# Performance work log

Measured on AMD Instinct MI355X. Metric: run time of the kernel, lower is better.

The kernel has to match this reference:

```python
import jax, jax.numpy as jnp
import numpy as np

B, N = 4, 20                        # batch, qubits
L = int(np.ceil(np.log2(N)))        # 5 layers, one 4x4 generator each


def setup_inputs():
    key = jax.random.key(0)
    k1, k2, k3, k4 = jax.random.split(key, 4)
    psi_re = jax.random.normal(k1, (B, 2 ** N), dtype=jnp.float32)
    psi_im = jax.random.normal(k2, (B, 2 ** N), dtype=jnp.float32)
    nrm = jnp.sqrt(jnp.sum(psi_re ** 2 + psi_im ** 2, axis=1, keepdims=True))
    psi_re, psi_im = psi_re / nrm, psi_im / nrm   # normalized quantum state
    H_re = jax.random.normal(k3, (L, 4, 4), dtype=jnp.float32)
    H_im = jax.random.normal(k4, (L, 4, 4), dtype=jnp.float32)
    return {"psi_re": psi_re, "psi_im": psi_im, "H_re": H_re, "H_im": H_im}


def _make_unitary(A):
    # torch.matrix_exp(A - A^H): expm of an anti-Hermitian generator via eigh
    G = A - A.conj().T
    w, V = jnp.linalg.eigh(-1j * G)            # G = i * Hermitian
    return (V * jnp.exp(1j * w)) @ V.conj().T  # expm(G), unitary


def _apply_gate(T, U4, axes):
    # contract 4x4 gate (reshaped [2,2,2,2]) onto two qubit axes of tensor T
    T = jnp.tensordot(U4, T, axes=((2, 3), axes))
    return jnp.moveaxis(T, (0, 1), axes)


def _gate_pairs(nq):
    pairs = [(2 * i, 2 * i + 1) for i in range(nq // 2)]
    if nq > 2:
        pairs += [(2 * i + 1, (2 * i + 2) % nq) for i in range(nq // 2)]
    return pairs


def _forward(psi_re, psi_im, H_re, H_im):
    psi = (psi_re + 1j * psi_im).astype(jnp.complex64).reshape((B,) + (2,) * N)
    H = (H_re + 1j * H_im).astype(jnp.complex64)
    state, is_dm, nq = psi, False, N
    for layer in range(L):
        U = _make_unitary(H[layer]).reshape(2, 2, 2, 2)
        Uc = U.conj()
        # _2local_conv: brick pattern of the same 2-qubit gate
        for (a, b) in _gate_pairs(nq):
            state = _apply_gate(state, U, (1 + a, 1 + b))
            if is_dm:  # density matrix: also apply U* on bra axes
                state = _apply_gate(state, Uc, (1 + nq + a, 1 + nq + b))
        # _2local_pool: measuring qubits 0..nq//2-1 with index shifting removes
        # the even-indexed qubits -> partial trace over them
        if nq >= 2:
            traced = [2 * i for i in range(nq // 2)]
            kept = [q for q in range(nq) if q not in traced]
            t, k = len(traced), len(kept)
            if is_dm:
                perm = (0,) + tuple(1 + q for q in kept) + tuple(1 + q for q in traced) \
                     + tuple(1 + nq + q for q in kept) + tuple(1 + nq + q for q in traced)
                r = jnp.transpose(state, perm).reshape(B, 2 ** k, 2 ** t, 2 ** k, 2 ** t)
                state = jnp.einsum('bitjt->bij', r).reshape((B,) + (2,) * k + (2,) * k)
            else:
                perm = (0,) + tuple(1 + q for q in traced) + tuple(1 + q for q in kept)
                p = jnp.transpose(state, perm).reshape(B, 2 ** t, 2 ** k)
                state = jnp.einsum('bti,btj->bij', p, p.conj()).reshape((B,) + (2,) * k + (2,) * k)
                is_dm = True
            nq = k
    # final state.measure(0): reduced 1-qubit density matrix, take P(outcome 0)
    r = state.reshape(B, 2, 2 ** (nq - 1), 2, 2 ** (nq - 1))
    rho0 = jnp.einsum('birjr->bij', r)
    return rho0[:, 0, 0].real


def reference(psi_re, psi_im, H_re, H_im):
    return _forward(psi_re, psi_im, H_re, H_im)
```

## Files before the change

kernel.cpp:

```cpp
#include <hip/hip_runtime.h>
#include <math.h>


typedef float cpx __attribute__((ext_vector_type(2)));

__device__ __forceinline__ cpx mkc(float x, float y) { cpx r; r.x = x; r.y = y; return r; }

__device__ __forceinline__ cpx cmul(cpx a, cpx b) {
  cpx r = a.xx * b;
  return __builtin_elementwise_fma(mkc(-a.y, a.y), b.yx, r);
}
__device__ __forceinline__ cpx cmadd(cpx acc, cpx a, cpx b) {
  acc = __builtin_elementwise_fma(a.xx, b, acc);
  return __builtin_elementwise_fma(mkc(-a.y, a.y), b.yx, acc);
}
__device__ __forceinline__ cpx cmaddc(cpx acc, cpx a, cpx b) {
  acc = __builtin_elementwise_fma(a.xx, mkc(b.x, -b.y), acc);
  return __builtin_elementwise_fma(a.yy, b.yx, acc);
}

__device__ __forceinline__ int pad(int e) { return e + (e >> 4); }
__device__ __forceinline__ int ins(int x, int p) {
  return ((x >> p) << (p + 1)) | (x & ((1 << p) - 1));
}

#define S_STR 36
#define T_STR 1153

__device__ __forceinline__ void gate4(cpx& v0, cpx& v1, cpx& v2, cpx& v3,
                                      const cpx (&U)[16]) {
  cpx n0 = cmul(U[0], v0);  n0 = cmadd(n0, U[1], v1);  n0 = cmadd(n0, U[2], v2);  n0 = cmadd(n0, U[3], v3);
  cpx n1 = cmul(U[4], v0);  n1 = cmadd(n1, U[5], v1);  n1 = cmadd(n1, U[6], v2);  n1 = cmadd(n1, U[7], v3);
  cpx n2 = cmul(U[8], v0);  n2 = cmadd(n2, U[9], v1);  n2 = cmadd(n2, U[10], v2); n2 = cmadd(n2, U[11], v3);
  cpx n3 = cmul(U[12], v0); n3 = cmadd(n3, U[13], v1); n3 = cmadd(n3, U[14], v2); n3 = cmadd(n3, U[15], v3);
  v0 = n0; v1 = n1; v2 = n2; v3 = n3;
}

template <int NG>
__device__ __forceinline__ void gate16n(cpx (&v)[16], const cpx (&U)[16]) {
#pragma unroll
  for (int g = 0; g < 4; g++)
    gate4(v[g * 4 + 0], v[g * 4 + 1], v[g * 4 + 2], v[g * 4 + 3], U);
#pragma unroll
  for (int lo = 0; lo < 4; lo++)
    gate4(v[lo], v[lo + 4], v[lo + 8], v[lo + 12], U);
  if (NG == 3) {
#pragma unroll
    for (int b3 = 0; b3 < 2; b3++)
#pragma unroll
      for (int b0 = 0; b0 < 2; b0++) {
        int j = b3 * 8 + b0;
        gate4(v[j], v[j + 2], v[j + 4], v[j + 6], U);
      }
  }
}

__device__ __forceinline__ void apply_gate_tile13(cpx* t, const cpx (&U)[16],
                                                  int pa, int pb, int tid) {
  int p0 = pa < pb ? pa : pb;
  int p1 = pa < pb ? pb : pa;
  int m0 = (1 << p0) - 1, m1 = (1 << p1) - 1;
  int ia = 1 << pa, ib = 1 << pb;
#pragma unroll
  for (int g = tid; g < 2048; g += 512) {
    int idx = ((g & ~m0) << 1) | (g & m0);
    idx = ((idx & ~m1) << 1) | (idx & m1);
    int e0 = pad(idx), e1 = pad(idx | ib), e2 = pad(idx | ia), e3 = pad(idx | ia | ib);
    cpx v0 = t[e0], v1 = t[e1], v2 = t[e2], v3 = t[e3];
    gate4(v0, v1, v2, v3, U);
    t[e0] = v0; t[e1] = v1; t[e2] = v2; t[e3] = v3;
  }
}

template <int NG>
__device__ __forceinline__ void phase4_f(cpx* t, const cpx (&U)[16],
                                         int q0, int q1, int q2, int q3,
                                         int o0, int o1, int o2, int o3, int tid) {
  int idx = ins(ins(ins(ins(tid, q0), q1), q2), q3);
  cpx v[16];
#pragma unroll
  for (int j = 0; j < 16; j++) {
    int off = ((j & 1) ? o0 : 0) + ((j & 2) ? o1 : 0) + ((j & 4) ? o2 : 0) + ((j & 8) ? o3 : 0);
    v[j] = t[pad(idx + off)];
  }
  gate16n<NG>(v, U);
#pragma unroll
  for (int j = 0; j < 16; j++) {
    int off = ((j & 1) ? o0 : 0) + ((j & 2) ? o1 : 0) + ((j & 4) ? o2 : 0) + ((j & 8) ? o3 : 0);
    t[pad(idx + off)] = v[j];
  }
}

template <int NG>
__device__ __forceinline__ void phase4_pool(cpx* w, const cpx (&U)[16],
                                            int a_lo, int a_hi, int c_lo, int c_hi,
                                            int o0, int o1, int o2, int o3, int tid) {
  int uu = tid & 7, ss = (tid >> 3) & 7, t_lo = tid >> 6;
  int u = ins(ins(uu, a_lo), a_hi);
  int s = ins(ins(ss, c_lo), c_hi);
  int base = t_lo * T_STR + s * S_STR + u;
  cpx v[16];
#pragma unroll
  for (int j = 0; j < 16; j++) {
    int off = ((j & 1) ? o0 : 0) + ((j & 2) ? o1 : 0) + ((j & 4) ? o2 : 0) + ((j & 8) ? o3 : 0);
    v[j] = w[base + off];
  }
  gate16n<NG>(v, U);
#pragma unroll
  for (int j = 0; j < 16; j++) {
    int off = ((j & 1) ? o0 : 0) + ((j & 2) ? o1 : 0) + ((j & 4) ? o2 : 0) + ((j & 8) ? o3 : 0);
    w[base + off] = v[j];
  }
}

__device__ __forceinline__ void pool_p3(cpx* w, const cpx (&U)[16], int tid) {
#pragma unroll
  for (int it = 0; it < 2; it++) {
    int h = tid + it * 512;
    int t_lo = h & 7, ss = (h >> 3) & 15, uu = (h >> 7) & 7;
    int base = t_lo * T_STR + (ss << 1) * S_STR + (uu << 2);
    cpx v[8];
    v[0] = w[base];          v[1] = w[base + 1];
    v[4] = w[base + 2];      v[5] = w[base + 3];
    v[2] = w[base + S_STR];      v[3] = w[base + S_STR + 1];
    v[6] = w[base + S_STR + 2];  v[7] = w[base + S_STR + 3];
    gate4(v[0], v[1], v[2], v[3], U);
    gate4(v[4], v[5], v[6], v[7], U);
    gate4(v[0], v[2], v[4], v[6], U);
    gate4(v[1], v[3], v[5], v[7], U);
    w[base] = v[0];          w[base + 1] = v[1];
    w[base + 2] = v[4];      w[base + 3] = v[5];
    w[base + S_STR] = v[2];      w[base + S_STR + 1] = v[3];
    w[base + S_STR + 2] = v[6];  w[base + S_STR + 3] = v[7];
  }
}

__device__ __forceinline__ cpx expm16(const float* __restrict__ Hre,
                                      const float* __restrict__ Him,
                                      int l, int l16) {
  int r = l16 >> 2, c = l16 & 3;
  double tr = (double)Hre[l * 16 + r * 4 + c] - (double)Hre[l * 16 + c * 4 + r];
  double ti = (double)Him[l * 16 + r * 4 + c] + (double)Him[l * 16 + c * 4 + r];
  double a = sqrt(tr * tr + ti * ti);
  a += __shfl_xor(a, 1, 16);
  a += __shfl_xor(a, 2, 16);
  double nrm = fmax(a, __shfl_xor(a, 4, 16));
  nrm = fmax(nrm, __shfl_xor(nrm, 8, 16));
  int s = 0;
  while (nrm > 0.25 && s < 60) { nrm *= 0.5; s++; }
  double sc = ldexp(1.0, -s);
  tr *= sc; ti *= sc;
  double id = (r == c) ? 1.0 : 0.0;
  double er = id, ei = 0.0, pr = id, pi = 0.0;
  for (int k = 1; k <= 16; k++) {
    double qr = 0.0, qi = 0.0;
#pragma unroll
    for (int m = 0; m < 4; m++) {
      double pmr = __shfl(pr, r * 4 + m, 16);
      double pmi = __shfl(pi, r * 4 + m, 16);
      double tmr = __shfl(tr, m * 4 + c, 16);
      double tmi = __shfl(ti, m * 4 + c, 16);
      qr = fma(pmr, tmr, fma(-pmi, tmi, qr));
      qi = fma(pmr, tmi, fma(pmi, tmr, qi));
    }
    double inv = 1.0 / (double)k;
    pr = qr * inv; pi = qi * inv;
    er += pr; ei += pi;
  }
  for (int it = 0; it < s; it++) {
    double qr = 0.0, qi = 0.0;
#pragma unroll
    for (int m = 0; m < 4; m++) {
      double amr = __shfl(er, r * 4 + m, 16);
      double ami = __shfl(ei, r * 4 + m, 16);
      double bmr = __shfl(er, m * 4 + c, 16);
      double bmi = __shfl(ei, m * 4 + c, 16);
      qr = fma(amr, bmr, fma(-ami, bmi, qr));
      qi = fma(amr, bmi, fma(ami, bmr, qi));
    }
    er = qr; ei = qi;
  }
  return mkc((float)er, (float)ei);
}

__global__ __launch_bounds__(256, 4) void l0_pass1(const float* __restrict__ pre,
                                                   const float* __restrict__ pim,
                                                   const float* __restrict__ Hre,
                                                   const float* __restrict__ Him,
                                                   cpx* __restrict__ Umat,
                                                   cpx* __restrict__ state) {
  extern __shared__ cpx tile[];
  __shared__ cpx Ush[16];
  int tid = threadIdx.x;
  int bid = blockIdx.x;
  int b = bid >> 8, hi = bid & 255;
  size_t base = ((size_t)b << 20) | ((size_t)hi << 12);
  for (int e4 = tid; e4 < 1024; e4 += 256) {
    int e = e4 << 2;
    float4 re = *(const float4*)&pre[base + e];
    float4 im = *(const float4*)&pim[base + e];
    int d = pad(e);
    tile[d] = mkc(re.x, im.x);
    tile[d + 1] = mkc(re.y, im.y);
    tile[d + 2] = mkc(re.z, im.z);
    tile[d + 3] = mkc(re.w, im.w);
  }
  {
    int wv = tid >> 6, g16 = (tid & 63) >> 4, l16 = tid & 15;
    int layer = (wv == 0) ? g16 : ((wv == 1 && g16 == 0) ? 4 : -1);
    if (layer == 0 || (bid == 0 && layer > 0)) {
      cpx ue = expm16(Hre, Him, layer, l16);
      if (layer == 0) Ush[l16] = ue;
      if (bid == 0) Umat[layer * 16 + l16] = ue;
    }
  }
  __syncthreads();
  cpx U[16];
#pragma unroll
  for (int k = 0; k < 16; k++) U[k] = Ush[k];
  phase4_f<3>(tile, U, 0, 1, 2, 3, 1, 2, 4, 8, tid);            __syncthreads();
  phase4_f<3>(tile, U, 4, 5, 6, 7, 16, 32, 64, 128, tid);       __syncthreads();
  phase4_f<3>(tile, U, 8, 9, 10, 11, 256, 512, 1024, 2048, tid);__syncthreads();
  phase4_f<2>(tile, U, 3, 4, 7, 8, 8, 16, 128, 256, tid);       __syncthreads();
  int hifix = ((hi & 1) << 4) | (((hi >> 1) & 1) << 16) | (((hi >> 2) & 1) << 6)
            | (((hi >> 3) & 1) << 17) | (((hi >> 4) & 1) << 5) | (((hi >> 5) & 1) << 18)
            | (((hi >> 6) & 1) << 7) | (((hi >> 7) & 1) << 19);
  size_t dbase = ((size_t)b << 20) | (unsigned)hifix;
  for (int e4 = tid; e4 < 1024; e4 += 256) {
    int le = e4;
    int d = ((le & 1) << 2) | (((le >> 1) & 1) << 3) | (((le >> 2) & 1) << 8)
          | (((le >> 3) & 1) << 12) | (((le >> 4) & 1) << 10) | (((le >> 5) & 1) << 13)
          | (((le >> 6) & 1) << 9) | (((le >> 7) & 1) << 14) | (((le >> 8) & 1) << 11)
          | (((le >> 9) & 1) << 15);
    int src = pad(e4 << 2);
    cpx x0 = tile[src], x1 = tile[src + 1], x2 = tile[src + 2], x3 = tile[src + 3];
    float4* dst = (float4*)&state[dbase + d];
    dst[0] = make_float4(x0.x, x0.y, x1.x, x1.y);
    dst[1] = make_float4(x2.x, x2.y, x3.x, x3.y);
  }
}

__global__ __launch_bounds__(512, 4) void l0_pass2(const cpx* __restrict__ Umat,
                                                   cpx* __restrict__ state) {
  extern __shared__ cpx tile[];
  int tid = threadIdx.x;
  int bid = blockIdx.x;
  int b = bid >> 7, mid = bid & 127;
  size_t base = ((size_t)b << 20) | ((size_t)mid << 8);
  cpx U[16];
#pragma unroll
  for (int k = 0; k < 16; k++) U[k] = Umat[k];
  for (int f = tid; f < 4096; f += 512) {
    int run = f >> 7, idx = f & 127;
    size_t a = base + ((size_t)run << 15) + ((size_t)idx << 1);
    float4 v = *(const float4*)&state[a];
    int d = pad(run * 256 + idx * 2);
    tile[d] = mkc(v.x, v.y);
    tile[d + 1] = mkc(v.z, v.w);
  }
  __syncthreads();
  phase4_f<3>(tile, U, 4, 6, 9, 10, 16, 512, 64, 1024, tid);    __syncthreads();
  phase4_f<3>(tile, U, 5, 7, 11, 12, 32, 2048, 128, 4096, tid); __syncthreads();
  phase4_f<2>(tile, U, 4, 5, 8, 10, 256, 16, 1024, 32, tid);    __syncthreads();
  apply_gate_tile13(tile, U, 0, 12, tid);                       __syncthreads();
  for (int f = tid; f < 4096; f += 512) {
    int run = f >> 7, idx = f & 127;
    size_t a = base + ((size_t)run << 15) + ((size_t)idx << 1);
    int d = pad(run * 256 + idx * 2);
    cpx x0 = tile[d], x1 = tile[d + 1];
    *(float4*)&state[a] = make_float4(x0.x, x0.y, x1.x, x1.y);
  }
}

__global__ __launch_bounds__(512, 4) void pool_l1(const cpx* __restrict__ Umat,
                                                  const cpx* __restrict__ state,
                                                  float4* __restrict__ partial) {
  extern __shared__ cpx w[];
  int tid = threadIdx.x;
  int bid = blockIdx.x;
  int b = bid >> 7, thi = bid & 127;
  size_t base = ((size_t)b << 20) | ((size_t)thi << 13);
  cpx U[16];
#pragma unroll
  for (int k = 0; k < 16; k++) U[k] = Umat[16 + k];
  for (int f = tid; f < 4096; f += 512) {
    int e = f << 1;
    float4 v = *(const float4*)&state[base + e];
    int u = (((e >> 8) & 1) << 1) | (((e >> 9) & 1) << 2) | (((e >> 4) & 1) << 3) | (((e >> 5) & 1) << 4);
    int s = ((e >> 2) & 1) | (((e >> 10) & 1) << 1) | (((e >> 11) & 1) << 2)
          | (((e >> 6) & 1) << 3) | (((e >> 7) & 1) << 4);
    int t = ((e >> 1) & 1) | (((e >> 3) & 1) << 1) | (((e >> 12) & 1) << 2);
    int c = t * T_STR + s * S_STR + u;
    w[c] = mkc(v.x, v.y);
    w[c + 1] = mkc(v.z, v.w);
  }
  __syncthreads();
  phase4_pool<3>(w, U, 3, 4, 3, 4, 8, 8 * S_STR, 16, 16 * S_STR, tid); __syncthreads();
  phase4_pool<3>(w, U, 1, 2, 1, 2, 2, 2 * S_STR, 4, 4 * S_STR, tid);   __syncthreads();
  pool_p3(w, U, tid);                                                  __syncthreads();
  phase4_pool<2>(w, U, 0, 3, 2, 4, 4 * S_STR, 8, 16 * S_STR, 1, tid);  __syncthreads();
  int wv = tid >> 6, lane = tid & 63;
  int u0 = (lane >> 3) << 2, v0 = (lane & 7) << 2;
  cpx acc[4][4];
#pragma unroll
  for (int i = 0; i < 4; i++)
#pragma unroll
    for (int j = 0; j < 4; j++) acc[i][j] = mkc(0.f, 0.f);
  {
    int tb = wv * T_STR;
#pragma unroll 4
    for (int s = 0; s < 32; s++) {
      int row = tb + s * S_STR;
      cpx x[4], y[4];
#pragma unroll
      for (int i = 0; i < 4; i++) { x[i] = w[row + u0 + i]; y[i] = w[row + v0 + i]; }
#pragma unroll
      for (int i = 0; i < 4; i++)
#pragma unroll
        for (int j = 0; j < 4; j++) acc[i][j] = cmaddc(acc[i][j], x[i], y[j]);
    }
  }
  __syncthreads();
#pragma unroll
  for (int i = 0; i < 4; i++)
#pragma unroll
    for (int j = 0; j < 4; j++)
      w[wv * 1024 + (u0 + i) * 32 + (v0 + j)] = acc[i][j];
  __syncthreads();
  {
    cpx s0 = mkc(0.f, 0.f), s1 = mkc(0.f, 0.f);
#pragma unroll
    for (int k = 0; k < 8; k++) {
      s0 += w[k * 1024 + 2 * tid];
      s1 += w[k * 1024 + 2 * tid + 1];
    }
    partial[((size_t)bid << 9) | tid] = make_float4(s0.x, s0.y, s1.x, s1.y);
  }
}

__global__ __launch_bounds__(256) void finish(const cpx* __restrict__ Umat,
                                              const float4* __restrict__ accv,
                                              float* __restrict__ out) {
  __shared__ cpx rho[1024];
  __shared__ cpx r3s[64];
  __shared__ cpx r4s[16];
  int tid = threadIdx.x;
  int b = blockIdx.x;
  float4* rf = (float4*)rho;
  for (int f = tid; f < 512; f += 256) {
    float4 acc = make_float4(0.f, 0.f, 0.f, 0.f);
#pragma unroll 8
    for (int h = 0; h < 128; h++) {
      float4 v = accv[(size_t)(b * 128 + h) * 512 + f];
      acc.x += v.x; acc.y += v.y; acc.z += v.z; acc.w += v.w;
    }
    rf[f] = acc;
  }
  __syncthreads();

  cpx U[16], Uc[16];
#pragma unroll
  for (int k = 0; k < 16; k++) { U[k] = Umat[32 + k]; Uc[k] = mkc(U[k].x, -U[k].y); }
  const int gl2[4][2] = {{4,3},{2,1},{3,2},{1,0}};
#pragma unroll
  for (int gi = 0; gi < 4; gi++) {
    int pa = gl2[gi][0], pb = gl2[gi][1];
    int p0 = pa < pb ? pa : pb, p1 = pa < pb ? pb : pa;
    int m0 = (1 << p0) - 1, m1 = (1 << p1) - 1;
    int ia = 1 << pa, ib = 1 << pb;
    {
      int j = tid >> 3, g = tid & 7;
      int idx = ((g & ~m0) << 1) | (g & m0);
      idx = ((idx & ~m1) << 1) | (idx & m1);
      cpx v0 = rho[idx * 32 + j], v1 = rho[(idx | ib) * 32 + j];
      cpx v2 = rho[(idx | ia) * 32 + j], v3 = rho[(idx | ia | ib) * 32 + j];
      gate4(v0, v1, v2, v3, U);
      rho[idx * 32 + j] = v0; rho[(idx | ib) * 32 + j] = v1;
      rho[(idx | ia) * 32 + j] = v2; rho[(idx | ia | ib) * 32 + j] = v3;
    }
    __syncthreads();
    {
      int i = tid >> 3, g = tid & 7;
      int idx = ((g & ~m0) << 1) | (g & m0);
      idx = ((idx & ~m1) << 1) | (idx & m1);
      cpx v0 = rho[i * 32 + idx], v1 = rho[i * 32 + (idx | ib)];
      cpx v2 = rho[i * 32 + (idx | ia)], v3 = rho[i * 32 + (idx | ia | ib)];
      gate4(v0, v1, v2, v3, Uc);
      rho[i * 32 + idx] = v0; rho[i * 32 + (idx | ib)] = v1;
      rho[i * 32 + (idx | ia)] = v2; rho[i * 32 + (idx | ia | ib)] = v3;
    }
    __syncthreads();
  }
  if (tid < 64) {
    int u = tid >> 3, v = tid & 7;
    cpx acc = mkc(0.f, 0.f);
#pragma unroll
    for (int s = 0; s < 4; s++) {
      int iu = ((s >> 1) << 4) | ((u >> 2) << 3) | ((s & 1) << 2) | (((u >> 1) & 1) << 1) | (u & 1);
      int iv = ((s >> 1) << 4) | ((v >> 2) << 3) | ((s & 1) << 2) | (((v >> 1) & 1) << 1) | (v & 1);
      cpx x = rho[iu * 32 + iv];
      acc.x += x.x; acc.y += x.y;
    }
    r3s[u * 8 + v] = acc;
  }
  __syncthreads();

#pragma unroll
  for (int k = 0; k < 16; k++) { U[k] = Umat[48 + k]; Uc[k] = mkc(U[k].x, -U[k].y); }
  const int gl3[2][2] = {{2,1},{1,0}};
#pragma unroll
  for (int gi = 0; gi < 2; gi++) {
    int pa = gl3[gi][0], pb = gl3[gi][1];
    int p0 = pa < pb ? pa : pb, p1 = pa < pb ? pb : pa;
    int m0 = (1 << p0) - 1, m1 = (1 << p1) - 1;
    int ia = 1 << pa, ib = 1 << pb;
    if (tid < 16) {
      int j = tid >> 1, g = tid & 1;
      int idx = ((g & ~m0) << 1) | (g & m0);
      idx = ((idx & ~m1) << 1) | (idx & m1);
      cpx v0 = r3s[idx * 8 + j], v1 = r3s[(idx | ib) * 8 + j];
      cpx v2 = r3s[(idx | ia) * 8 + j], v3 = r3s[(idx | ia | ib) * 8 + j];
      gate4(v0, v1, v2, v3, U);
      r3s[idx * 8 + j] = v0; r3s[(idx | ib) * 8 + j] = v1;
      r3s[(idx | ia) * 8 + j] = v2; r3s[(idx | ia | ib) * 8 + j] = v3;
    }
    __syncthreads();
    if (tid < 16) {
      int i = tid >> 1, g = tid & 1;
      int idx = ((g & ~m0) << 1) | (g & m0);
      idx = ((idx & ~m1) << 1) | (idx & m1);
      cpx v0 = r3s[i * 8 + idx], v1 = r3s[i * 8 + (idx | ib)];
      cpx v2 = r3s[i * 8 + (idx | ia)], v3 = r3s[i * 8 + (idx | ia | ib)];
      gate4(v0, v1, v2, v3, Uc);
      r3s[i * 8 + idx] = v0; r3s[i * 8 + (idx | ib)] = v1;
      r3s[i * 8 + (idx | ia)] = v2; r3s[i * 8 + (idx | ia | ib)] = v3;
    }
    __syncthreads();
  }
  if (tid < 16) {
    int u = tid >> 2, v = tid & 3;
    cpx acc = mkc(0.f, 0.f);
#pragma unroll
    for (int s = 0; s < 2; s++) {
      cpx x = r3s[((s << 2) | u) * 8 + ((s << 2) | v)];
      acc.x += x.x; acc.y += x.y;
    }
    r4s[u * 4 + v] = acc;
  }
  __syncthreads();

#pragma unroll
  for (int k = 0; k < 16; k++) { U[k] = Umat[64 + k]; Uc[k] = mkc(U[k].x, -U[k].y); }
  if (tid < 4) {
    int j = tid;
    cpx v0 = r4s[0 * 4 + j], v1 = r4s[1 * 4 + j], v2 = r4s[2 * 4 + j], v3 = r4s[3 * 4 + j];
    gate4(v0, v1, v2, v3, U);
    r4s[0 * 4 + j] = v0; r4s[1 * 4 + j] = v1; r4s[2 * 4 + j] = v2; r4s[3 * 4 + j] = v3;
  }
  __syncthreads();
  if (tid < 4) {
    int i = tid;
    cpx v0 = r4s[i * 4 + 0], v1 = r4s[i * 4 + 1], v2 = r4s[i * 4 + 2], v3 = r4s[i * 4 + 3];
    gate4(v0, v1, v2, v3, Uc);
    r4s[i * 4 + 0] = v0; r4s[i * 4 + 1] = v1; r4s[i * 4 + 2] = v2; r4s[i * 4 + 3] = v3;
  }
  __syncthreads();
  if (tid == 0) out[b] = r4s[0].x + r4s[10].x;
}

extern "C" void kernel_launch(void* const* d_in, const int* in_sizes, int n_in,
                              void* d_out, int out_size, void* d_ws, size_t ws_size,
                              hipStream_t stream) {
  const float* psi_re = (const float*)d_in[0];
  const float* psi_im = (const float*)d_in[1];
  const float* H_re = (const float*)d_in[2];
  const float* H_im = (const float*)d_in[3];
  float* out = (float*)d_out;

  char* ws = (char*)d_ws;
  cpx* Umat = (cpx*)ws;
  cpx* state = (cpx*)(ws + 4096);
  float4* partial = (float4*)(ws + 4096 + ((size_t)1 << 25));

  const size_t LDS_P1 = 4352 * sizeof(cpx);
  const size_t LDS_L0 = 8704 * sizeof(cpx);
  const size_t LDS_POOL = 8 * T_STR * sizeof(cpx);

  hipLaunchKernelGGL(l0_pass1, dim3(1024), dim3(256), LDS_P1, stream,
                     psi_re, psi_im, H_re, H_im, Umat, state);
  hipLaunchKernelGGL(l0_pass2, dim3(512), dim3(512), LDS_L0, stream,
                     (const cpx*)Umat, state);
  hipLaunchKernelGGL(pool_l1, dim3(512), dim3(512), LDS_POOL, stream,
                     (const cpx*)Umat, (const cpx*)state, partial);
  hipLaunchKernelGGL(finish, dim3(4), dim3(256), 0, stream,
                     (const cpx*)Umat, (const float4*)partial, out);
}
```

Before: 175.5 us.

## Enlarge pass1 tiles to 8K elements and batch global loads before LDS stores

l0_pass1 now handles 8192-element tiles with 512 threads instead of 4096 with 256, so the grid halves and the output bit permutation gains one more tile-local bit. Across all three big kernels, the global loads are first gathered into register arrays and then written to LDS (likewise on the stores), which raises memory-level parallelism per thread. The cost is higher register pressure and, in pass1, a doubled LDS footprint that may cut occupancy.

Result: slower. 183.0 us (+4.3%).

```diff
diff --git a/kernel.cpp b/kernel.cpp
--- a/kernel.cpp
+++ b/kernel.cpp
@@ -183,7 +183,7 @@
   return mkc((float)er, (float)ei);
 }
 
-__global__ __launch_bounds__(256, 4) void l0_pass1(const float* __restrict__ pre,
+__global__ __launch_bounds__(512, 4) void l0_pass1(const float* __restrict__ pre,
                                                    const float* __restrict__ pim,
                                                    const float* __restrict__ Hre,
                                                    const float* __restrict__ Him,
@@ -193,17 +193,23 @@
   __shared__ cpx Ush[16];
   int tid = threadIdx.x;
   int bid = blockIdx.x;
-  int b = bid >> 8, hi = bid & 255;
-  size_t base = ((size_t)b << 20) | ((size_t)hi << 12);
-  for (int e4 = tid; e4 < 1024; e4 += 256) {
-    int e = e4 << 2;
-    float4 re = *(const float4*)&pre[base + e];
-    float4 im = *(const float4*)&pim[base + e];
+  int b = bid >> 7, hi = bid & 127;
+  size_t base = ((size_t)b << 20) | ((size_t)hi << 13);
+  float4 re[4], im[4];
+#pragma unroll
+  for (int k = 0; k < 4; k++) {
+    int e = (tid + (k << 9)) << 2;
+    re[k] = *(const float4*)&pre[base + e];
+    im[k] = *(const float4*)&pim[base + e];
+  }
+#pragma unroll
+  for (int k = 0; k < 4; k++) {
+    int e = (tid + (k << 9)) << 2;
     int d = pad(e);
-    tile[d] = mkc(re.x, im.x);
-    tile[d + 1] = mkc(re.y, im.y);
-    tile[d + 2] = mkc(re.z, im.z);
-    tile[d + 3] = mkc(re.w, im.w);
+    tile[d]     = mkc(re[k].x, im[k].x);
+    tile[d + 1] = mkc(re[k].y, im[k].y);
+    tile[d + 2] = mkc(re[k].z, im[k].z);
+    tile[d + 3] = mkc(re[k].w, im[k].w);
   }
   {
     int wv = tid >> 6, g16 = (tid & 63) >> 4, l16 = tid & 15;
@@ -222,21 +228,27 @@
   phase4_f<3>(tile, U, 4, 5, 6, 7, 16, 32, 64, 128, tid);       __syncthreads();
   phase4_f<3>(tile, U, 8, 9, 10, 11, 256, 512, 1024, 2048, tid);__syncthreads();
   phase4_f<2>(tile, U, 3, 4, 7, 8, 8, 16, 128, 256, tid);       __syncthreads();
-  int hifix = ((hi & 1) << 4) | (((hi >> 1) & 1) << 16) | (((hi >> 2) & 1) << 6)
-            | (((hi >> 3) & 1) << 17) | (((hi >> 4) & 1) << 5) | (((hi >> 5) & 1) << 18)
-            | (((hi >> 6) & 1) << 7) | (((hi >> 7) & 1) << 19);
+  int hifix = ((hi & 1) << 16) | (((hi >> 1) & 1) << 6) | (((hi >> 2) & 1) << 17)
+            | (((hi >> 3) & 1) << 5) | (((hi >> 4) & 1) << 18) | (((hi >> 5) & 1) << 7)
+            | (((hi >> 6) & 1) << 19);
   size_t dbase = ((size_t)b << 20) | (unsigned)hifix;
-  for (int e4 = tid; e4 < 1024; e4 += 256) {
-    int le = e4;
+  cpx x[16];
+#pragma unroll
+  for (int k = 0; k < 4; k++) {
+    int src = pad((tid + (k << 9)) << 2);
+    x[4 * k + 0] = tile[src];     x[4 * k + 1] = tile[src + 1];
+    x[4 * k + 2] = tile[src + 2]; x[4 * k + 3] = tile[src + 3];
+  }
+#pragma unroll
+  for (int k = 0; k < 4; k++) {
+    int le = tid + (k << 9);
     int d = ((le & 1) << 2) | (((le >> 1) & 1) << 3) | (((le >> 2) & 1) << 8)
           | (((le >> 3) & 1) << 12) | (((le >> 4) & 1) << 10) | (((le >> 5) & 1) << 13)
           | (((le >> 6) & 1) << 9) | (((le >> 7) & 1) << 14) | (((le >> 8) & 1) << 11)
-          | (((le >> 9) & 1) << 15);
-    int src = pad(e4 << 2);
-    cpx x0 = tile[src], x1 = tile[src + 1], x2 = tile[src + 2], x3 = tile[src + 3];
+          | (((le >> 9) & 1) << 15) | (((le >> 10) & 1) << 4);
     float4* dst = (float4*)&state[dbase + d];
-    dst[0] = make_float4(x0.x, x0.y, x1.x, x1.y);
-    dst[1] = make_float4(x2.x, x2.y, x3.x, x3.y);
+    dst[0] = make_float4(x[4 * k].x, x[4 * k].y, x[4 * k + 1].x, x[4 * k + 1].y);
+    dst[1] = make_float4(x[4 * k + 2].x, x[4 * k + 2].y, x[4 * k + 3].x, x[4 * k + 3].y);
   }
 }
 
@@ -250,25 +262,43 @@
   cpx U[16];
 #pragma unroll
   for (int k = 0; k < 16; k++) U[k] = Umat[k];
-  for (int f = tid; f < 4096; f += 512) {
-    int run = f >> 7, idx = f & 127;
-    size_t a = base + ((size_t)run << 15) + ((size_t)idx << 1);
-    float4 v = *(const float4*)&state[a];
-    int d = pad(run * 256 + idx * 2);
-    tile[d] = mkc(v.x, v.y);
-    tile[d + 1] = mkc(v.z, v.w);
+  {
+    float4 v[8];
+#pragma unroll
+    for (int k = 0; k < 8; k++) {
+      int f = tid + (k << 9);
+      int run = f >> 7, idx = f & 127;
+      v[k] = *(const float4*)&state[base + ((size_t)run << 15) + ((size_t)idx << 1)];
+    }
+#pragma unroll
+    for (int k = 0; k < 8; k++) {
+      int f = tid + (k << 9);
+      int d = pad((f >> 7) * 256 + (f & 127) * 2);
+      tile[d] = mkc(v[k].x, v[k].y);
+      tile[d + 1] = mkc(v[k].z, v[k].w);
+    }
   }
   __syncthreads();
   phase4_f<3>(tile, U, 4, 6, 9, 10, 16, 512, 64, 1024, tid);    __syncthreads();
   phase4_f<3>(tile, U, 5, 7, 11, 12, 32, 2048, 128, 4096, tid); __syncthreads();
   phase4_f<2>(tile, U, 4, 5, 8, 10, 256, 16, 1024, 32, tid);    __syncthreads();
   apply_gate_tile13(tile, U, 0, 12, tid);                       __syncthreads();
-  for (int f = tid; f < 4096; f += 512) {
-    int run = f >> 7, idx = f & 127;
-    size_t a = base + ((size_t)run << 15) + ((size_t)idx << 1);
-    int d = pad(run * 256 + idx * 2);
-    cpx x0 = tile[d], x1 = tile[d + 1];
-    *(float4*)&state[a] = make_float4(x0.x, x0.y, x1.x, x1.y);
+  {
+    cpx y[16];
+#pragma unroll
+    for (int k = 0; k < 8; k++) {
+      int f = tid + (k << 9);
+      int d = pad((f >> 7) * 256 + (f & 127) * 2);
+      y[2 * k] = tile[d];
+      y[2 * k + 1] = tile[d + 1];
+    }
+#pragma unroll
+    for (int k = 0; k < 8; k++) {
+      int f = tid + (k << 9);
+      int run = f >> 7, idx = f & 127;
+      size_t a = base + ((size_t)run << 15) + ((size_t)idx << 1);
+      *(float4*)&state[a] = make_float4(y[2 * k].x, y[2 * k].y, y[2 * k + 1].x, y[2 * k + 1].y);
+    }
   }
 }
 
@@ -283,16 +313,24 @@
   cpx U[16];
 #pragma unroll
   for (int k = 0; k < 16; k++) U[k] = Umat[16 + k];
-  for (int f = tid; f < 4096; f += 512) {
-    int e = f << 1;
-    float4 v = *(const float4*)&state[base + e];
-    int u = (((e >> 8) & 1) << 1) | (((e >> 9) & 1) << 2) | (((e >> 4) & 1) << 3) | (((e >> 5) & 1) << 4);
-    int s = ((e >> 2) & 1) | (((e >> 10) & 1) << 1) | (((e >> 11) & 1) << 2)
-          | (((e >> 6) & 1) << 3) | (((e >> 7) & 1) << 4);
-    int t = ((e >> 1) & 1) | (((e >> 3) & 1) << 1) | (((e >> 12) & 1) << 2);
-    int c = t * T_STR + s * S_STR + u;
-    w[c] = mkc(v.x, v.y);
-    w[c + 1] = mkc(v.z, v.w);
+  {
+    float4 v[8];
+#pragma unroll
+    for (int k = 0; k < 8; k++) {
+      int e = (tid + (k << 9)) << 1;
+      v[k] = *(const float4*)&state[base + e];
+    }
+#pragma unroll
+    for (int k = 0; k < 8; k++) {
+      int e = (tid + (k << 9)) << 1;
+      int u = (((e >> 8) & 1) << 1) | (((e >> 9) & 1) << 2) | (((e >> 4) & 1) << 3) | (((e >> 5) & 1) << 4);
+      int s = ((e >> 2) & 1) | (((e >> 10) & 1) << 1) | (((e >> 11) & 1) << 2)
+            | (((e >> 6) & 1) << 3) | (((e >> 7) & 1) << 4);
+      int t = ((e >> 1) & 1) | (((e >> 3) & 1) << 1) | (((e >> 12) & 1) << 2);
+      int c = t * T_STR + s * S_STR + u;
+      w[c] = mkc(v[k].x, v[k].y);
+      w[c + 1] = mkc(v[k].z, v[k].w);
+    }
   }
   __syncthreads();
   phase4_pool<3>(w, U, 3, 4, 3, 4, 8, 8 * S_STR, 16, 16 * S_STR, tid); __syncthreads();
@@ -482,11 +520,10 @@
   cpx* state = (cpx*)(ws + 4096);
   float4* partial = (float4*)(ws + 4096 + ((size_t)1 << 25));
 
-  const size_t LDS_P1 = 4352 * sizeof(cpx);
   const size_t LDS_L0 = 8704 * sizeof(cpx);
   const size_t LDS_POOL = 8 * T_STR * sizeof(cpx);
 
-  hipLaunchKernelGGL(l0_pass1, dim3(1024), dim3(256), LDS_P1, stream,
+  hipLaunchKernelGGL(l0_pass1, dim3(512), dim3(512), LDS_L0, stream,
                      psi_re, psi_im, H_re, H_im, Umat, state);
   hipLaunchKernelGGL(l0_pass2, dim3(512), dim3(512), LDS_L0, stream,
                      (const cpx*)Umat, state);
```
